# Optimization experiments

Hardware: AMD Instinct MI355X
Metric: run time of the kernel (lower is better)

## Reference

```python
import jax, jax.numpy as jnp
import numpy as np

N, IN_DIM, HID, OUT, E = 20000, 1024, 512, 128, 160000


def _xavier(key, fan_out, fan_in):
    a = (6.0 / (fan_in + fan_out)) ** 0.5
    return jax.random.uniform(key, (fan_out, fan_in), jnp.float32, -a, a)


def setup_inputs() -> dict:
    key = jax.random.key(0)
    ks = jax.random.split(key, 8)
    features = jax.random.normal(ks[0], (N, IN_DIM), jnp.float32)
    edge_index = jax.random.randint(ks[1], (2, E), 0, N, jnp.int64)
    W1 = _xavier(ks[2], HID, IN_DIM)   # conv1.lin.weight [out,in]
    b1 = jnp.zeros((HID,), jnp.float32)
    W2 = _xavier(ks[3], OUT, HID)      # conv2.lin.weight
    b2 = jnp.zeros((OUT,), jnp.float32)
    b3 = jnp.zeros((HID,), jnp.float32)  # conv3 bias (weight tied = W2.T)
    b4 = jnp.zeros((IN_DIM,), jnp.float32)  # conv4 bias (weight tied = W1.T)
    head1 = _xavier(ks[4], OUT, OUT)
    return dict(features=features, edge_index=edge_index, W1=W1, b1=b1,
                W2=W2, b2=b2, b3=b3, b4=b4, head1=head1)


def _gcn_conv(x, W, b, src, dst, norm, n):
    # GCNConv: transform then symmetric-normalized neighbor aggregation
    h = x @ W.T                       # [N, out]
    msg = h[src] * norm[:, None]      # [E', out] gathered + scaled
    out = jax.ops.segment_sum(msg, dst, num_segments=n)
    return out + b


def reference(features, edge_index, W1, b1, W2, b2, b3, b4, head1):
    n = features.shape[0]
    loops = jnp.arange(n, dtype=edge_index.dtype)
    src = jnp.concatenate([edge_index[0], loops])  # add self-loops
    dst = jnp.concatenate([edge_index[1], loops])
    deg = jax.ops.segment_sum(jnp.ones_like(dst, dtype=features.dtype), dst,
                              num_segments=n)
    dinv = jnp.where(deg > 0, deg ** -0.5, 0.0)
    norm = dinv[src] * dinv[dst]

    h1 = _gcn_conv(features, W1, b1, src, dst, norm, n)
    h2 = _gcn_conv(h1, W2, b2, src, dst, norm, n)
    z = h2 @ head1
    # tied weights: conv3.W = W2^T, conv4.W = W1^T
    h3 = _gcn_conv(z, W2.T, b3, src, dst, norm, n)
    h4 = _gcn_conv(h3, W1.T, b4, src, dst, norm, n)
    return z, h2, h4
```

## Files before the change

kernel.cpp:

```cpp
#include <hip/hip_runtime.h>

typedef short   short8  __attribute__((ext_vector_type(8)));
typedef unsigned short ushort8 __attribute__((ext_vector_type(8)));
typedef float   floatx4 __attribute__((ext_vector_type(4)));

__device__ __forceinline__ float bf2f(unsigned short h) {
    unsigned int u = ((unsigned int)h) << 16;
    return __builtin_bit_cast(float, u);
}
__device__ __forceinline__ unsigned short f2bf(float f) {
    unsigned int u = __builtin_bit_cast(unsigned int, f);
    u += 0x7fffu + ((u >> 16) & 1u);
    return (unsigned short)(u >> 16);
}


__global__ __launch_bounds__(256) void k_detect_f32(const unsigned short* __restrict__ X,
                                                    int nPairs, int* __restrict__ flags) {
    int i = blockIdx.x * 256 + threadIdx.x;
    if (i < nPairs) {
        unsigned short w = X[2 * i];
        if ((w & 0x7F80u) == 0x7F80u) atomicOr(&flags[0], 1);
    }
}

__global__ __launch_bounds__(256) void k_detect_i32(const int* __restrict__ ei,
                                                    int E, int* __restrict__ flags) {
    int i = blockIdx.x * 256 + threadIdx.x;
    if (i < E) {
        if (ei[2 * i + 1] != 0) atomicOr(&flags[1], 1);
    }
}


__global__ __launch_bounds__(256) void k_cvt_f32(const void* __restrict__ in,
                                                 float* __restrict__ out, int n,
                                                 const int* __restrict__ flags) {
    int i = blockIdx.x * 256 + threadIdx.x;
    if (i < n)
        out[i] = flags[0] ? ((const float*)in)[i] : bf2f(((const unsigned short*)in)[i]);
}

__global__ __launch_bounds__(256) void k_cvt8(const void* __restrict__ in,
                                              unsigned short* __restrict__ out,
                                              long n8, const int* __restrict__ flags) {
    long i = (long)blockIdx.x * 256 + threadIdx.x;
    if (i >= n8) return;
    ushort8 o;
    if (flags[0]) {
        const floatx4* f = (const floatx4*)in + i * 2;
        floatx4 a = f[0], b = f[1];
#pragma unroll
        for (int j = 0; j < 4; j++) { o[j] = f2bf(a[j]); o[4 + j] = f2bf(b[j]); }
    } else {
        o = *((const ushort8*)in + i);
    }
    *((ushort8*)out + i) = o;
}

__global__ __launch_bounds__(256) void k_tcvt(const void* __restrict__ in,
                                              unsigned short* __restrict__ out,
                                              int R, int C, const int* __restrict__ flags) {
    int idx = blockIdx.x * 256 + threadIdx.x;
    if (idx >= R * C) return;
    int r = idx / C, c = idx - r * C;
    unsigned short v = flags[0] ? f2bf(((const float*)in)[idx])
                                : ((const unsigned short*)in)[idx];
    out[(long)c * R + r] = v;
}


__global__ __launch_bounds__(256) void k_count(const int* __restrict__ ei, int E, int n,
                                               const int* __restrict__ flags,
                                               int* __restrict__ deg) {
    int e = blockIdx.x * 256 + threadIdx.x;
    if (e >= E) return;
    int sh = (flags[1] == 0) ? 1 : 0;
    int d = ei[(long)(E + e) << sh];
    if ((unsigned)d < (unsigned)n) atomicAdd(&deg[d], 1);
}

__global__ __launch_bounds__(256) void k_dinv(const int* __restrict__ deg,
                                              float* __restrict__ dinv, int n) {
    int i = blockIdx.x * 256 + threadIdx.x;
    if (i < n) dinv[i] = rsqrtf((float)(deg[i] + 1));
}

__global__ __launch_bounds__(1024) void k_scan(const int* __restrict__ deg,
                                               int* __restrict__ row_start,
                                               int* __restrict__ cursor, int n) {
    __shared__ int sums[1024];
    int t = threadIdx.x;
    int CH = (n + 1 + 1023) / 1024;
    int base = t * CH;
    int s = 0;
    for (int i = 0; i < CH; i++) {
        int idx = base + i;
        if (idx < n) s += deg[idx];
    }
    sums[t] = s;
    __syncthreads();
    for (int off = 1; off < 1024; off <<= 1) {
        int v = (t >= off) ? sums[t - off] : 0;
        __syncthreads();
        if (t >= off) sums[t] += v;
        __syncthreads();
    }
    int run = (t > 0) ? sums[t - 1] : 0;
    for (int i = 0; i < CH; i++) {
        int idx = base + i;
        if (idx < n) {
            row_start[idx] = run;
            cursor[idx] = run;
            run += deg[idx];
        } else if (idx == n) {
            row_start[n] = run;
        }
    }
}

__global__ __launch_bounds__(256) void k_fill(const int* __restrict__ ei, int E, int n,
                                              const int* __restrict__ flags,
                                              int* __restrict__ cursor,
                                              int* __restrict__ csr) {
    int e = blockIdx.x * 256 + threadIdx.x;
    if (e >= E) return;
    int sh = (flags[1] == 0) ? 1 : 0;
    int s = ei[(long)e << sh];
    int d = ei[(long)(E + e) << sh];
    if ((unsigned)d >= (unsigned)n || (unsigned)s >= (unsigned)n) return;
    int p = atomicAdd(&cursor[d], 1);
    csr[p] = s;
}


template <int BN>
__global__ __launch_bounds__(256, 3) void gemm_nt(const unsigned short* __restrict__ A,
                                               const unsigned short* __restrict__ Bt,
                                               void* __restrict__ Cv, long coff,
                                               const float* __restrict__ bias,
                                               int M, int N, int K, int finalOut,
                                               const int* __restrict__ flags) {
    constexpr int BM = 128, BK = 32, LDT = 40;
    constexpr int JR = BN / 16;
    __shared__ unsigned short sA[BM * LDT];
    __shared__ unsigned short sB[BN * LDT];
    const bool of32 = finalOut && flags[0];
    const bool hasb = bias != nullptr;
    const int t = threadIdx.x;

    const int GX = gridDim.x;
    const int nwg = GX * gridDim.y;
    const int orig = blockIdx.y * GX + blockIdx.x;
    const int q8 = nwg >> 3, r8 = nwg & 7;
    const int xcd = orig & 7, cidx = orig >> 3;
    const int swz = (xcd < r8 ? xcd * (q8 + 1) : r8 * (q8 + 1) + (xcd - r8) * q8) + cidx;
    const int m0 = (swz / GX) * BM;
    const int n0 = (swz % GX) * BN;

    const int w = t >> 6;
    const int lane = t & 63;
    const int id = lane & 15;
    const int q = lane >> 4;

    floatx4 acc[2][JR];
#pragma unroll
    for (int s = 0; s < 2; s++)
#pragma unroll
        for (int j = 0; j < JR; j++) acc[s][j] = (floatx4)0.0f;

    const int ar = t >> 2;
    const int ac = (t & 3) * 8;

    const unsigned short* pa0 = A + (long)min(m0 + ar, M - 1) * K + ac;
    const unsigned short* pa1 = A + (long)min(m0 + ar + 64, M - 1) * K + ac;
    const unsigned short* pb0 = Bt + (long)min(n0 + ar, N - 1) * K + ac;
    const unsigned short* pb1 = Bt + (long)min(n0 + ar + ((BN == 128) ? 64 : 0), N - 1) * K + ac;

    ushort8 va0 = *(const ushort8*)(pa0);
    ushort8 va1 = *(const ushort8*)(pa1);
    ushort8 vb0 = *(const ushort8*)(pb0);
    ushort8 vb1;
    if (BN == 128) vb1 = *(const ushort8*)(pb1);

    for (int k0 = 0; k0 < K; k0 += BK) {
        __syncthreads();
        *(ushort8*)(sA + ar * LDT + ac) = va0;
        *(ushort8*)(sA + (ar + 64) * LDT + ac) = va1;
        *(ushort8*)(sB + ar * LDT + ac) = vb0;
        if (BN == 128)
            *(ushort8*)(sB + (ar + 64) * LDT + ac) = vb1;
        __syncthreads();

        if (k0 + BK < K) {
            va0 = *(const ushort8*)(pa0 + k0 + BK);
            va1 = *(const ushort8*)(pa1 + k0 + BK);
            vb0 = *(const ushort8*)(pb0 + k0 + BK);
            if (BN == 128) vb1 = *(const ushort8*)(pb1 + k0 + BK);
        }

        short8 afrag[2], bfrag[JR];
#pragma unroll
        for (int s = 0; s < 2; s++)
            afrag[s] = *(const short8*)(sA + (32 * w + 16 * s + id) * LDT + q * 8);
#pragma unroll
        for (int j = 0; j < JR; j++)
            bfrag[j] = *(const short8*)(sB + (16 * j + id) * LDT + q * 8);
#pragma unroll
        for (int s = 0; s < 2; s++)
#pragma unroll
            for (int j = 0; j < JR; j++)
                acc[s][j] = __builtin_amdgcn_mfma_f32_16x16x32_bf16(
                    afrag[s], bfrag[j], acc[s][j], 0, 0, 0);
    }

#pragma unroll
    for (int s = 0; s < 2; s++)
#pragma unroll
        for (int j = 0; j < JR; j++) {
            int col = n0 + 16 * j + id;
            float bv = hasb ? bias[col] : 0.0f;
#pragma unroll
            for (int r = 0; r < 4; r++) {
                int row = m0 + 32 * w + 16 * s + q * 4 + r;
                if (row < M) {
                    float v = acc[s][j][r] + bv;
                    if (of32) ((float*)Cv)[coff + (long)row * N + col] = v;
                    else ((unsigned short*)Cv)[coff + (long)row * N + col] = f2bf(v);
                }
            }
        }
}


template <int D>
__global__ __launch_bounds__(256) void k_agg(const unsigned short* __restrict__ T,
                                             const int* __restrict__ rs,
                                             const int* __restrict__ csr,
                                             const float* __restrict__ dinv,
                                             const float* __restrict__ bias,
                                             unsigned short* __restrict__ O, int n) {
    constexpr int TPN = D / 8;
    constexpr int NPB = 256 / TPN;
    int lt = threadIdx.x % TPN;
    int node = blockIdx.x * NPB + threadIdx.x / TPN;
    if (node >= n) return;
    int off = lt * 8;
    float acc[8];
#pragma unroll
    for (int i = 0; i < 8; i++) acc[i] = 0.0f;
    int beg = rs[node], end = rs[node + 1];
    for (int j = beg; j < end; j++) {
        int s = csr[j];
        if ((unsigned)s >= (unsigned)n) continue;
        float wgt = dinv[s];
        ushort8 v = *(const ushort8*)(T + (long)s * D + off);
#pragma unroll
        for (int i = 0; i < 8; i++) acc[i] += wgt * bf2f(v[i]);
    }
    float di = dinv[node];
    ushort8 sv = *(const ushort8*)(T + (long)node * D + off);
    ushort8 o;
#pragma unroll
    for (int i = 0; i < 8; i++) {
        float r = di * (acc[i] + di * bf2f(sv[i])) + (bias ? bias[off + i] : 0.0f);
        o[i] = f2bf(r);
    }
    *(ushort8*)(O + (long)node * D + off) = o;
}


__global__ __launch_bounds__(256) void k_out(const unsigned short* __restrict__ z,
                                             const unsigned short* __restrict__ h2,
                                             void* __restrict__ out, int nOut,
                                             const int* __restrict__ flags) {
    int i = blockIdx.x * 256 + threadIdx.x;
    if (i >= 2 * nOut) return;
    unsigned short v = (i < nOut) ? z[i] : h2[i - nOut];
    if (flags[0]) ((float*)out)[i] = bf2f(v);
    else ((unsigned short*)out)[i] = v;
}


extern "C" void kernel_launch(void* const* d_in, const int* in_sizes, int n_in,
                              void* d_out, int out_size, void* d_ws, size_t ws_size,
                              hipStream_t stream) {
    const int IN  = in_sizes[7];
    const int HID = in_sizes[3];
    const int OUT = in_sizes[5];
    const int Nn  = in_sizes[0] / IN;
    const int E   = in_sizes[1] / 2;

    const void* X   = d_in[0];
    const int*  ei  = (const int*)d_in[1];
    const void* W1  = d_in[2];
    const void* b1  = d_in[3];
    const void* W2  = d_in[4];
    const void* b2  = d_in[5];
    const void* b3  = d_in[6];
    const void* b4  = d_in[7];
    const void* Hd1 = d_in[8];

    char* base = (char*)d_ws;
    size_t o = 0;
    auto carve = [&](size_t bytes) -> char* {
        char* p = base + o;
        o = (o + bytes + 255) & ~(size_t)255;
        return p;
    };
    int*   flags  = (int*)carve(2 * 4);
    int*   deg    = (int*)carve((size_t)Nn * 4);
    int*   rowst  = (int*)carve((size_t)(Nn + 1) * 4);
    int*   cursor = (int*)carve((size_t)Nn * 4);
    float* dinv   = (float*)carve((size_t)Nn * 4);
    int*   csr    = (int*)carve((size_t)E * 4);
    float* biasf  = (float*)carve((size_t)(HID + OUT + HID + IN) * 4);
    float* bc1 = biasf, *bc2 = biasf + HID, *bc3 = biasf + HID + OUT,
         *bc4 = biasf + HID + OUT + HID;
    unsigned short* W1t  = (unsigned short*)carve((size_t)IN * HID * 2);
    unsigned short* W2t  = (unsigned short*)carve((size_t)HID * OUT * 2);
    unsigned short* H1t  = (unsigned short*)carve((size_t)OUT * OUT * 2);
    unsigned short* W1c  = (unsigned short*)carve((size_t)HID * IN * 2);
    unsigned short* W2c  = (unsigned short*)carve((size_t)OUT * HID * 2);
    unsigned short* Xb   = (unsigned short*)carve((size_t)Nn * IN * 2);
    unsigned short* t1   = (unsigned short*)carve((size_t)Nn * HID * 2);
    unsigned short* h1   = (unsigned short*)carve((size_t)Nn * HID * 2);
    unsigned short* h3   = (unsigned short*)carve((size_t)Nn * HID * 2);
    unsigned short* t2   = (unsigned short*)carve((size_t)Nn * OUT * 2);
    unsigned short* h2ws = (unsigned short*)carve((size_t)Nn * OUT * 2);
    unsigned short* zws  = (unsigned short*)carve((size_t)Nn * OUT * 2);

    hipMemsetAsync(flags, 0, 8, stream);
    hipMemsetAsync(deg, 0, (size_t)Nn * 4, stream);
    int nPairs = 1 << 20;
    k_detect_f32<<<(nPairs + 255) / 256, 256, 0, stream>>>((const unsigned short*)X, nPairs, flags);
    k_detect_i32<<<(E + 255) / 256, 256, 0, stream>>>(ei, E, flags);

    k_cvt_f32<<<(HID + 255) / 256, 256, 0, stream>>>(b1, bc1, HID, flags);
    k_cvt_f32<<<(OUT + 255) / 256, 256, 0, stream>>>(b2, bc2, OUT, flags);
    k_cvt_f32<<<(HID + 255) / 256, 256, 0, stream>>>(b3, bc3, HID, flags);
    k_cvt_f32<<<(IN + 255) / 256, 256, 0, stream>>>(b4, bc4, IN, flags);

    k_tcvt<<<(HID * IN + 255) / 256, 256, 0, stream>>>(W1, W1t, HID, IN, flags);
    k_tcvt<<<(OUT * HID + 255) / 256, 256, 0, stream>>>(W2, W2t, OUT, HID, flags);
    k_tcvt<<<(OUT * OUT + 255) / 256, 256, 0, stream>>>(Hd1, H1t, OUT, OUT, flags);

    {
        long n8x = (long)Nn * IN / 8;
        k_cvt8<<<(int)((n8x + 255) / 256), 256, 0, stream>>>(X, Xb, n8x, flags);
        long n8w1 = (long)HID * IN / 8;
        k_cvt8<<<(int)((n8w1 + 255) / 256), 256, 0, stream>>>(W1, W1c, n8w1, flags);
        long n8w2 = (long)OUT * HID / 8;
        k_cvt8<<<(int)((n8w2 + 255) / 256), 256, 0, stream>>>(W2, W2c, n8w2, flags);
    }

    k_count<<<(E + 255) / 256, 256, 0, stream>>>(ei, E, Nn, flags, deg);
    k_dinv<<<(Nn + 255) / 256, 256, 0, stream>>>(deg, dinv, Nn);
    k_scan<<<1, 1024, 0, stream>>>(deg, rowst, cursor, Nn);
    k_fill<<<(E + 255) / 256, 256, 0, stream>>>(ei, E, Nn, flags, cursor, csr);

    dim3 blk(256);
    auto ggrid = [&](int Ncols, int bn) { return dim3((Ncols + bn - 1) / bn, (Nn + 127) / 128); };
    const long zOff = 0, h2Off = (long)Nn * OUT, h4Off = (long)Nn * OUT * 2;

    gemm_nt<64><<<ggrid(HID, 64), blk, 0, stream>>>(Xb, W1c, t1, 0, nullptr, Nn, HID, IN, 0, flags);
    k_agg<512><<<(Nn * 64 + 255) / 256, blk, 0, stream>>>(t1, rowst, csr, dinv, bc1, h1, Nn);

    gemm_nt<64><<<ggrid(OUT, 64), blk, 0, stream>>>(h1, W2c, t2, 0, nullptr, Nn, OUT, HID, 0, flags);
    k_agg<128><<<(Nn * 16 + 255) / 256, blk, 0, stream>>>(t2, rowst, csr, dinv, bc2, h2ws, Nn);

    gemm_nt<64><<<ggrid(OUT, 64), blk, 0, stream>>>(h2ws, H1t, zws, 0, nullptr, Nn, OUT, OUT, 0, flags);

    k_agg<128><<<(Nn * 16 + 255) / 256, blk, 0, stream>>>(zws, rowst, csr, dinv, nullptr, t2, Nn);
    gemm_nt<64><<<ggrid(HID, 64), blk, 0, stream>>>(t2, W2t, h3, 0, bc3, Nn, HID, OUT, 0, flags);

    k_agg<512><<<(Nn * 64 + 255) / 256, blk, 0, stream>>>(h3, rowst, csr, dinv, nullptr, t1, Nn);
    gemm_nt<128><<<ggrid(IN, 128), blk, 0, stream>>>(t1, W1t, d_out, h4Off, bc4, Nn, IN, HID, 1, flags);

    k_out<<<(2 * (int)h2Off + 255) / 256, blk, 0, stream>>>(zws, h2ws, d_out, (int)h2Off, flags);
}
```

Before: 564.0 us.

## Double-buffer GEMM LDS tiles, vectorize epilogue, add BM=64 variant for narrow GEMMs

The GEMM now keeps two LDS buffers and writes the next K-tile while computing on the current one, which needs only one barrier per step instead of two. MFMA operands are swapped so each lane holds four consecutive output columns, letting the epilogue write vectorized bf16x4 or float4 stores and load the bias as a vector. A BM template parameter adds a 64-row tile, used for the two small OUT-column GEMMs to raise the block count, and launch bounds allow more waves for BN=64. The cost is double the LDS per block, which may limit occupancy, and the new K loop assumes K is a multiple of 64.

```diff
diff --git a/kernel.cpp b/kernel.cpp
--- a/kernel.cpp
+++ b/kernel.cpp
@@ -2,6 +2,7 @@
 
 typedef short   short8  __attribute__((ext_vector_type(8)));
 typedef unsigned short ushort8 __attribute__((ext_vector_type(8)));
+typedef unsigned short bf4     __attribute__((ext_vector_type(4)));
 typedef float   floatx4 __attribute__((ext_vector_type(4)));
 
 __device__ __forceinline__ float bf2f(unsigned short h) {
@@ -134,17 +135,19 @@
 }
 
 
-template <int BN>
-__global__ __launch_bounds__(256, 3) void gemm_nt(const unsigned short* __restrict__ A,
-                                               const unsigned short* __restrict__ Bt,
-                                               void* __restrict__ Cv, long coff,
-                                               const float* __restrict__ bias,
-                                               int M, int N, int K, int finalOut,
-                                               const int* __restrict__ flags) {
-    constexpr int BM = 128, BK = 32, LDT = 40;
+template <int BM, int BN>
+__global__ __launch_bounds__(256, (BN == 128 ? 3 : 4))
+void gemm_nt(const unsigned short* __restrict__ A,
+             const unsigned short* __restrict__ Bt,
+             void* __restrict__ Cv, long coff,
+             const float* __restrict__ bias,
+             int M, int N, int K, int finalOut,
+             const int* __restrict__ flags) {
+    constexpr int BK = 32, LDT = 40;
     constexpr int JR = BN / 16;
-    __shared__ unsigned short sA[BM * LDT];
-    __shared__ unsigned short sB[BN * LDT];
+    constexpr int SM = BM / 64;
+    __shared__ unsigned short sA[2][BM * LDT];
+    __shared__ unsigned short sB[2][BN * LDT];
     const bool of32 = finalOut && flags[0];
     const bool hasb = bias != nullptr;
     const int t = threadIdx.x;
@@ -163,9 +166,9 @@
     const int id = lane & 15;
     const int q = lane >> 4;
 
-    floatx4 acc[2][JR];
-#pragma unroll
-    for (int s = 0; s < 2; s++)
+    floatx4 acc[SM][JR];
+#pragma unroll
+    for (int s = 0; s < SM; s++)
 #pragma unroll
         for (int j = 0; j < JR; j++) acc[s][j] = (floatx4)0.0f;
 
@@ -173,63 +176,81 @@
     const int ac = (t & 3) * 8;
 
     const unsigned short* pa0 = A + (long)min(m0 + ar, M - 1) * K + ac;
-    const unsigned short* pa1 = A + (long)min(m0 + ar + 64, M - 1) * K + ac;
+    const unsigned short* pa1 = (SM == 2)
+        ? A + (long)min(m0 + ar + 64, M - 1) * K + ac : pa0;
     const unsigned short* pb0 = Bt + (long)min(n0 + ar, N - 1) * K + ac;
-    const unsigned short* pb1 = Bt + (long)min(n0 + ar + ((BN == 128) ? 64 : 0), N - 1) * K + ac;
-
-    ushort8 va0 = *(const ushort8*)(pa0);
-    ushort8 va1 = *(const ushort8*)(pa1);
-    ushort8 vb0 = *(const ushort8*)(pb0);
-    ushort8 vb1;
-    if (BN == 128) vb1 = *(const ushort8*)(pb1);
-
-    for (int k0 = 0; k0 < K; k0 += BK) {
+    const unsigned short* pb1 = (JR == 8)
+        ? Bt + (long)min(n0 + ar + 64, N - 1) * K + ac : pb0;
+
+    {
+        ushort8 va0 = *(const ushort8*)(pa0);
+        ushort8 va1; if (SM == 2) va1 = *(const ushort8*)(pa1);
+        ushort8 vb0 = *(const ushort8*)(pb0);
+        ushort8 vb1; if (JR == 8) vb1 = *(const ushort8*)(pb1);
+        *(ushort8*)(sA[0] + ar * LDT + ac) = va0;
+        if (SM == 2) *(ushort8*)(sA[0] + (ar + 64) * LDT + ac) = va1;
+        *(ushort8*)(sB[0] + ar * LDT + ac) = vb0;
+        if (JR == 8) *(ushort8*)(sB[0] + (ar + 64) * LDT + ac) = vb1;
         __syncthreads();
-        *(ushort8*)(sA + ar * LDT + ac) = va0;
-        *(ushort8*)(sA + (ar + 64) * LDT + ac) = va1;
-        *(ushort8*)(sB + ar * LDT + ac) = vb0;
-        if (BN == 128)
-            *(ushort8*)(sB + (ar + 64) * LDT + ac) = vb1;
-        __syncthreads();
-
-        if (k0 + BK < K) {
-            va0 = *(const ushort8*)(pa0 + k0 + BK);
-            va1 = *(const ushort8*)(pa1 + k0 + BK);
-            vb0 = *(const ushort8*)(pb0 + k0 + BK);
-            if (BN == 128) vb1 = *(const ushort8*)(pb1 + k0 + BK);
+    }
+
+    auto STEP = [&](int k0, const unsigned short* sAr, const unsigned short* sBr,
+                    unsigned short* sAw, unsigned short* sBw, bool last) {
+        ushort8 na0, na1, nb0, nb1;
+        if (!last) {
+            na0 = *(const ushort8*)(pa0 + k0 + BK);
+            if (SM == 2) na1 = *(const ushort8*)(pa1 + k0 + BK);
+            nb0 = *(const ushort8*)(pb0 + k0 + BK);
+            if (JR == 8) nb1 = *(const ushort8*)(pb1 + k0 + BK);
         }
-
-        short8 afrag[2], bfrag[JR];
-#pragma unroll
-        for (int s = 0; s < 2; s++)
-            afrag[s] = *(const short8*)(sA + (32 * w + 16 * s + id) * LDT + q * 8);
+        short8 afrag[SM], bfrag[JR];
+#pragma unroll
+        for (int s = 0; s < SM; s++)
+            afrag[s] = *(const short8*)(sAr + ((SM == 2 ? 32 * w + 16 * s : 16 * w) + id) * LDT + q * 8);
 #pragma unroll
         for (int j = 0; j < JR; j++)
-            bfrag[j] = *(const short8*)(sB + (16 * j + id) * LDT + q * 8);
-#pragma unroll
-        for (int s = 0; s < 2; s++)
+            bfrag[j] = *(const short8*)(sBr + (16 * j + id) * LDT + q * 8);
+#pragma unroll
+        for (int s = 0; s < SM; s++)
 #pragma unroll
             for (int j = 0; j < JR; j++)
                 acc[s][j] = __builtin_amdgcn_mfma_f32_16x16x32_bf16(
-                    afrag[s], bfrag[j], acc[s][j], 0, 0, 0);
-    }
-
-#pragma unroll
-    for (int s = 0; s < 2; s++)
-#pragma unroll
-        for (int j = 0; j < JR; j++) {
-            int col = n0 + 16 * j + id;
-            float bv = hasb ? bias[col] : 0.0f;
-#pragma unroll
-            for (int r = 0; r < 4; r++) {
-                int row = m0 + 32 * w + 16 * s + q * 4 + r;
-                if (row < M) {
-                    float v = acc[s][j][r] + bv;
-                    if (of32) ((float*)Cv)[coff + (long)row * N + col] = v;
-                    else ((unsigned short*)Cv)[coff + (long)row * N + col] = f2bf(v);
+                    bfrag[j], afrag[s], acc[s][j], 0, 0, 0);
+        if (!last) {
+            *(ushort8*)(sAw + ar * LDT + ac) = na0;
+            if (SM == 2) *(ushort8*)(sAw + (ar + 64) * LDT + ac) = na1;
+            *(ushort8*)(sBw + ar * LDT + ac) = nb0;
+            if (JR == 8) *(ushort8*)(sBw + (ar + 64) * LDT + ac) = nb1;
+            __syncthreads();
+        }
+    };
+
+    for (int k0 = 0; k0 < K; k0 += 2 * BK) {
+        STEP(k0, sA[0], sB[0], sA[1], sB[1], false);
+        STEP(k0 + BK, sA[1], sB[1], sA[0], sB[0], k0 + 2 * BK >= K);
+    }
+
+#pragma unroll
+    for (int s = 0; s < SM; s++) {
+        const int row = m0 + (SM == 2 ? 32 * w + 16 * s : 16 * w) + id;
+        if (row < M) {
+#pragma unroll
+            for (int j = 0; j < JR; j++) {
+                const int colb = n0 + 16 * j + 4 * q;
+                floatx4 v = acc[s][j];
+                if (hasb) v = v + *(const floatx4*)(bias + colb);
+                const long off = coff + (long)row * N + colb;
+                if (of32) {
+                    *(floatx4*)((float*)Cv + off) = v;
+                } else {
+                    bf4 o;
+#pragma unroll
+                    for (int r = 0; r < 4; r++) o[r] = f2bf(v[r]);
+                    *(bf4*)((unsigned short*)Cv + off) = o;
                 }
             }
         }
+    }
 }
 
 
@@ -360,22 +381,24 @@
     k_fill<<<(E + 255) / 256, 256, 0, stream>>>(ei, E, Nn, flags, cursor, csr);
 
     dim3 blk(256);
-    auto ggrid = [&](int Ncols, int bn) { return dim3((Ncols + bn - 1) / bn, (Nn + 127) / 128); };
-    const long zOff = 0, h2Off = (long)Nn * OUT, h4Off = (long)Nn * OUT * 2;
-
-    gemm_nt<64><<<ggrid(HID, 64), blk, 0, stream>>>(Xb, W1c, t1, 0, nullptr, Nn, HID, IN, 0, flags);
+    auto ggrid = [&](int Ncols, int bn, int bm) {
+        return dim3((Ncols + bn - 1) / bn, (Nn + bm - 1) / bm);
+    };
+    const long h2Off = (long)Nn * OUT, h4Off = (long)Nn * OUT * 2;
+
+    gemm_nt<128, 64><<<ggrid(HID, 64, 128), blk, 0, stream>>>(Xb, W1c, t1, 0, nullptr, Nn, HID, IN, 0, flags);
     k_agg<512><<<(Nn * 64 + 255) / 256, blk, 0, stream>>>(t1, rowst, csr, dinv, bc1, h1, Nn);
 
-    gemm_nt<64><<<ggrid(OUT, 64), blk, 0, stream>>>(h1, W2c, t2, 0, nullptr, Nn, OUT, HID, 0, flags);
+    gemm_nt<64, 64><<<ggrid(OUT, 64, 64), blk, 0, stream>>>(h1, W2c, t2, 0, nullptr, Nn, OUT, HID, 0, flags);
     k_agg<128><<<(Nn * 16 + 255) / 256, blk, 0, stream>>>(t2, rowst, csr, dinv, bc2, h2ws, Nn);
 
-    gemm_nt<64><<<ggrid(OUT, 64), blk, 0, stream>>>(h2ws, H1t, zws, 0, nullptr, Nn, OUT, OUT, 0, flags);
+    gemm_nt<64, 64><<<ggrid(OUT, 64, 64), blk, 0, stream>>>(h2ws, H1t, zws, 0, nullptr, Nn, OUT, OUT, 0, flags);
 
     k_agg<128><<<(Nn * 16 + 255) / 256, blk, 0, stream>>>(zws, rowst, csr, dinv, nullptr, t2, Nn);
-    gemm_nt<64><<<ggrid(HID, 64), blk, 0, stream>>>(t2, W2t, h3, 0, bc3, Nn, HID, OUT, 0, flags);
+    gemm_nt<128, 64><<<ggrid(HID, 64, 128), blk, 0, stream>>>(t2, W2t, h3, 0, bc3, Nn, HID, OUT, 0, flags);
 
     k_agg<512><<<(Nn * 64 + 255) / 256, blk, 0, stream>>>(h3, rowst, csr, dinv, nullptr, t1, Nn);
-    gemm_nt<128><<<ggrid(IN, 128), blk, 0, stream>>>(t1, W1t, d_out, h4Off, bc4, Nn, IN, HID, 1, flags);
+    gemm_nt<128, 128><<<ggrid(IN, 128, 128), blk, 0, stream>>>(t1, W1t, d_out, h4Off, bc4, Nn, IN, HID, 1, flags);
 
     k_out<<<(2 * (int)h2Off + 255) / 256, blk, 0, stream>>>(zws, h2ws, d_out, (int)h2Off, flags);
 }
```

Measured after the change: 546.0 us. 1.03x faster.
